# Kernel optimization log

Measured on AMD Instinct MI355X. Metric: run time of the kernel, lower is better.

Reference implementation:

```python
import jax, jax.numpy as jnp
import numpy as np

N, E, D, G, C = 50000, 800000, 128, 64, 2
SCALE = 1.0 / np.sqrt(D).astype(np.float32)


def setup_inputs() -> dict:
    key = jax.random.key(0)
    ks = jax.random.split(key, 32)
    inp = {
        "x": jax.random.normal(ks[0], (N, D), dtype=jnp.float32),
        "edge_index": jax.random.randint(ks[1], (2, E), 0, N),
        "batch": jnp.sort(jax.random.randint(ks[2], (N,), 0, G)),
    }
    i = 3
    for l in range(2):
        for nm in ("Wq", "Wk", "Wv", "Ws"):
            inp[f"{nm}{l}"] = jax.random.normal(ks[i], (D, D), dtype=jnp.float32) * 0.05
            i += 1
        for nm in ("bq", "bk", "bv", "bs"):
            inp[f"{nm}{l}"] = jnp.zeros((D,), dtype=jnp.float32)
    inp["Wc1"] = jax.random.normal(ks[i], (D // 2, D), dtype=jnp.float32) * 0.05
    inp["bc1"] = jnp.zeros((D // 2,), dtype=jnp.float32)
    inp["Wc2"] = jax.random.normal(ks[i + 1], (C, D // 2), dtype=jnp.float32) * 0.05
    inp["bc2"] = jnp.zeros((C,), dtype=jnp.float32)
    return inp


def _transformer_conv(x, src, dst, Wq, bq, Wk, bk, Wv, bv, Ws, bs):
    # PyG TransformerConv, heads=1, concat=True, root_weight=True, beta=False.
    q = x @ Wq.T + bq            # [N, D] node-level projections, then gather per edge
    k = x @ Wk.T + bk
    v = x @ Wv.T + bv
    alpha = jnp.sum(q[dst] * k[src], axis=-1) * SCALE          # [E]
    # segment softmax over incoming edges of each target node
    m = jax.ops.segment_max(alpha, dst, num_segments=N)         # [N]
    ea = jnp.exp(alpha - m[dst])
    denom = jax.ops.segment_sum(ea, dst, num_segments=N)        # [N]
    w = ea / denom[dst]                                         # [E]
    out = jax.ops.segment_sum(v[src] * w[:, None], dst, num_segments=N)  # [N, D]
    return out + x @ Ws.T + bs   # skip connection (lin_skip)


def reference(x, edge_index, batch,
              Wq0, bq0, Wk0, bk0, Wv0, bv0, Ws0, bs0,
              Wq1, bq1, Wk1, bk1, Wv1, bv1, Ws1, bs1,
              Wc1, bc1, Wc2, bc2):
    src, dst = edge_index[0], edge_index[1]
    h = _transformer_conv(x, src, dst, Wq0, bq0, Wk0, bk0, Wv0, bv0, Ws0, bs0)
    h = jax.nn.relu(h)  # dropout is a no-op in eval mode
    h = _transformer_conv(h, src, dst, Wq1, bq1, Wk1, bk1, Wv1, bv1, Ws1, bs1)
    h = jax.nn.relu(h)
    # global mean pool over graphs
    sums = jax.ops.segment_sum(h, batch, num_segments=G)        # [G, D]
    cnts = jax.ops.segment_sum(jnp.ones((h.shape[0],), h.dtype), batch, num_segments=G)
    pooled = sums / jnp.maximum(cnts, 1.0)[:, None]
    # classifier MLP: [D -> D//2 -> C]
    z = jax.nn.relu(pooled @ Wc1.T + bc1)
    return z @ Wc2.T + bc2
```

## Files before the change

### kernel.cpp

```cpp
#include <hip/hip_runtime.h>
#include <math.h>

typedef __bf16 bf16x8 __attribute__((ext_vector_type(8)));
typedef float  f32x4  __attribute__((ext_vector_type(4)));
typedef float  f32x2  __attribute__((ext_vector_type(2)));
typedef unsigned short ushort_t;
typedef unsigned short ushort8 __attribute__((ext_vector_type(8)));

constexpr int Nn = 50000;
constexpr int Ee = 800000;
constexpr int Dd = 128;
constexpr int Gg = 64;
constexpr float SCALE = 0.08838834764831845f;
constexpr float QS    = 16.0f;
constexpr float ISC   = SCALE / (QS * QS);

constexpr int CPAD = 16;

__device__ inline ushort_t f2bf(float f) {
    unsigned u = __float_as_uint(f);
    unsigned r = (u + 0x7FFF + ((u >> 16) & 1)) >> 16;
    return (ushort_t)r;
}
__device__ inline float bf2f(ushort_t b) { return __uint_as_float(((unsigned)b) << 16); }

__device__ inline char q_i8(float f) {
    int v = (int)rintf(f * QS);
    v = max(-127, min(127, v));
    return (char)v;
}

__device__ inline int xcd_group(int b, int n) {
    int q = n >> 3, r = n & 7;
    int xcd = b & 7, idx = b >> 3;
    int base = (xcd < r) ? xcd * (q + 1) : r * (q + 1) + (xcd - r) * q;
    return base + idx;
}


constexpr int EB8 = (Ee + 2047) / 2048;
constexpr int NBD = (Nn + 255) / 256;
constexpr int CWB = 64;
constexpr int N8  = Nn * Dd / 8;
constexpr int CXB = N8 / 256;

__global__ __launch_bounds__(256) void prep_kernel(
    const int* __restrict__ dst, int* __restrict__ counts, int* __restrict__ rank,
    const int* __restrict__ batch, int* __restrict__ startg, int* __restrict__ endg,
    const float* w0, const float* w1, const float* w2, const float* w3,
    const float* w4, const float* w5, const float* w6, const float* w7,
    ushort_t* __restrict__ Wfh, ushort_t* __restrict__ Wfl,
    const float* __restrict__ x, ushort_t* __restrict__ Xh, ushort_t* __restrict__ Xl) {
    int b = blockIdx.x;
    if (b < EB8) {
        int e0 = (b * 256 + threadIdx.x) * 8;
        if (e0 >= Ee) return;
        int4 d0 = *(const int4*)(dst + e0);
        int4 d1 = *(const int4*)(dst + e0 + 4);
        int r0 = atomicAdd(&counts[d0.x * CPAD], 1);
        int r1 = atomicAdd(&counts[d0.y * CPAD], 1);
        int r2 = atomicAdd(&counts[d0.z * CPAD], 1);
        int r3 = atomicAdd(&counts[d0.w * CPAD], 1);
        int r4 = atomicAdd(&counts[d1.x * CPAD], 1);
        int r5 = atomicAdd(&counts[d1.y * CPAD], 1);
        int r6 = atomicAdd(&counts[d1.z * CPAD], 1);
        int r7 = atomicAdd(&counts[d1.w * CPAD], 1);
        *(int4*)(rank + e0)     = (int4){r0, r1, r2, r3};
        *(int4*)(rank + e0 + 4) = (int4){r4, r5, r6, r7};
    } else if (b < EB8 + NBD) {
        int n = (b - EB8) * 256 + threadIdx.x;
        if (n >= Nn) return;
        int g = batch[n];
        if (n == Nn - 1 || batch[n + 1] != g) endg[g] = n + 1;
        if (n == 0 || batch[n - 1] != g) startg[g] = n;
    } else if (b < EB8 + NBD + CWB) {
        const float* ws[8] = {w0, w1, w2, w3, w4, w5, w6, w7};
        int b2 = b - (EB8 + NBD);
        int m = b2 >> 3;
        int tt = (b2 & 7) * 256 + threadIdx.x;
        int lane = tt & 63;
        int ln = lane & 15, quad = lane >> 4;
        int n = (tt >> 9) * 32 + ((tt >> 8) & 1) * 16 + ln;
        int k0 = ((tt >> 6) & 3) * 32 + quad * 8;
        const float* srcp = ws[m] + n * 128 + k0;
        float4 a = *(const float4*)(srcp);
        float4 bb = *(const float4*)(srcp + 4);
        float e[8] = {a.x, a.y, a.z, a.w, bb.x, bb.y, bb.z, bb.w};
        ushort8 h, l;
#pragma unroll
        for (int j = 0; j < 8; ++j) {
            h[j] = f2bf(e[j]);
            l[j] = f2bf(e[j] - bf2f(h[j]));
        }
        size_t o = (size_t)m * 16384 + (size_t)tt * 8;
        *(ushort8*)(Wfh + o) = h;
        *(ushort8*)(Wfl + o) = l;
    } else {
        int i = (b - (EB8 + NBD + CWB)) * 256 + threadIdx.x;
        if (i >= N8) return;
        float4 xa = ((const float4*)x)[i * 2];
        float4 xb = ((const float4*)x)[i * 2 + 1];
        float e[8] = {xa.x, xa.y, xa.z, xa.w, xb.x, xb.y, xb.z, xb.w};
        ushort8 h, l;
#pragma unroll
        for (int j = 0; j < 8; ++j) {
            h[j] = f2bf(e[j]);
            l[j] = f2bf(e[j] - bf2f(h[j]));
        }
        ((ushort8*)Xh)[i] = h;
        ((ushort8*)Xl)[i] = l;
    }
}


__global__ __launch_bounds__(256) void scan1_kernel(const int* __restrict__ counts,
                                                    int* __restrict__ offsets,
                                                    int* __restrict__ blockSums) {
    __shared__ int sh[256];
    int i = blockIdx.x * 256 + threadIdx.x;
    int v = (i < Nn) ? counts[i * CPAD] : 0;
    sh[threadIdx.x] = v;
    __syncthreads();
    for (int off = 1; off < 256; off <<= 1) {
        int t = (threadIdx.x >= off) ? sh[threadIdx.x - off] : 0;
        __syncthreads();
        sh[threadIdx.x] += t;
        __syncthreads();
    }
    if (i < Nn) offsets[i] = sh[threadIdx.x] - v;
    if (threadIdx.x == 255) blockSums[blockIdx.x] = sh[255];
}

__global__ __launch_bounds__(256) void scan2_kernel(int* __restrict__ blockSums, int nb) {
    __shared__ int sh[256];
    int t = threadIdx.x;
    int v = (t < nb) ? blockSums[t] : 0;
    sh[t] = v;
    __syncthreads();
    for (int off = 1; off < 256; off <<= 1) {
        int u = (t >= off) ? sh[t - off] : 0;
        __syncthreads();
        sh[t] += u;
        __syncthreads();
    }
    if (t < nb) blockSums[t] = sh[t] - v;
}


constexpr int XS = 136;
constexpr int NT = (Nn + 127) / 128;

__device__ __attribute__((always_inline)) void gemm_body(int bx, int which,
    const ushort_t* __restrict__ Xh, const ushort_t* __restrict__ Xl,
    const ushort_t* __restrict__ Wfh, const ushort_t* __restrict__ Wfl,
    int lw,
    const float* __restrict__ b0, const float* __restrict__ b1,
    const float* __restrict__ b2, const float* __restrict__ b3,
    char* __restrict__ Oq, char* __restrict__ Okv,
    ushort_t* __restrict__ Os) {
    __shared__ ushort_t XhS[32 * XS];
    __shared__ ushort_t XlS[32 * XS];
    const ushort_t* wfh = Wfh + (size_t)(lw + which) * 16384;
    const ushort_t* wfl = Wfl + (size_t)(lw + which) * 16384;
    const float* bias = (which == 0) ? b0 : (which == 1) ? b1 : (which == 2) ? b2 : b3;
    char* O8 = (which == 0) ? Oq : (which == 1) ? Okv : Okv + 128;
    int   o8str = (which == 0) ? 128 : 256;

    int w = threadIdx.x >> 6;
    int lane = threadIdx.x & 63;
    int quad = lane >> 4, ln = lane & 15;
    int n0 = w * 32;

    bf16x8 bh[2][4], bl[2][4];
#pragma unroll
    for (int ct = 0; ct < 2; ++ct)
#pragma unroll
        for (int kc = 0; kc < 4; ++kc) {
            int off = (w * 512 + ct * 256 + kc * 64 + lane) * 8;
            bh[ct][kc] = *(const bf16x8*)(wfh + off);
            bl[ct][kc] = *(const bf16x8*)(wfl + off);
        }
    float bias0 = bias[n0 + ln];
    float bias1 = bias[n0 + 16 + ln];

    int rowBase = bx * 128;
    int trow = threadIdx.x >> 4;
    int tcol = (threadIdx.x & 15) * 8;

    for (int chunk = 0; chunk < 4; ++chunk) {
        int cbase = rowBase + chunk * 32;
        __syncthreads();
#pragma unroll
        for (int rr = 0; rr < 2; ++rr) {
            int lrow = trow + rr * 16;
            int grow = min(cbase + lrow, Nn - 1);
            *(ushort8*)(&XhS[lrow * XS + tcol]) =
                *(const ushort8*)(Xh + (size_t)grow * 128 + tcol);
            *(ushort8*)(&XlS[lrow * XS + tcol]) =
                *(const ushort8*)(Xl + (size_t)grow * 128 + tcol);
        }
        __syncthreads();

#pragma unroll
        for (int rt = 0; rt < 2; ++rt) {
            const ushort_t* ph = &XhS[(rt * 16 + ln) * XS + quad * 8];
            const ushort_t* pl = &XlS[(rt * 16 + ln) * XS + quad * 8];
            bf16x8 ah[4], al[4];
#pragma unroll
            for (int kc = 0; kc < 4; ++kc) {
                ah[kc] = *(const bf16x8*)(ph + kc * 32);
                al[kc] = *(const bf16x8*)(pl + kc * 32);
            }
            f32x4 acc00 = {0.f,0.f,0.f,0.f}, acc01 = {0.f,0.f,0.f,0.f};
            f32x4 acc10 = {0.f,0.f,0.f,0.f}, acc11 = {0.f,0.f,0.f,0.f};
#pragma unroll
            for (int kc = 0; kc < 2; ++kc) {
                int k2 = kc + 2;
                acc00 = __builtin_amdgcn_mfma_f32_16x16x32_bf16(ah[kc], bh[0][kc], acc00, 0, 0, 0);
                acc01 = __builtin_amdgcn_mfma_f32_16x16x32_bf16(ah[kc], bh[1][kc], acc01, 0, 0, 0);
                acc10 = __builtin_amdgcn_mfma_f32_16x16x32_bf16(ah[k2], bh[0][k2], acc10, 0, 0, 0);
                acc11 = __builtin_amdgcn_mfma_f32_16x16x32_bf16(ah[k2], bh[1][k2], acc11, 0, 0, 0);
                acc00 = __builtin_amdgcn_mfma_f32_16x16x32_bf16(ah[kc], bl[0][kc], acc00, 0, 0, 0);
                acc01 = __builtin_amdgcn_mfma_f32_16x16x32_bf16(ah[kc], bl[1][kc], acc01, 0, 0, 0);
                acc10 = __builtin_amdgcn_mfma_f32_16x16x32_bf16(ah[k2], bl[0][k2], acc10, 0, 0, 0);
                acc11 = __builtin_amdgcn_mfma_f32_16x16x32_bf16(ah[k2], bl[1][k2], acc11, 0, 0, 0);
                acc00 = __builtin_amdgcn_mfma_f32_16x16x32_bf16(al[kc], bh[0][kc], acc00, 0, 0, 0);
                acc01 = __builtin_amdgcn_mfma_f32_16x16x32_bf16(al[kc], bh[1][kc], acc01, 0, 0, 0);
                acc10 = __builtin_amdgcn_mfma_f32_16x16x32_bf16(al[k2], bh[0][k2], acc10, 0, 0, 0);
                acc11 = __builtin_amdgcn_mfma_f32_16x16x32_bf16(al[k2], bh[1][k2], acc11, 0, 0, 0);
            }
            int m0 = cbase + rt * 16;
            int orow0 = m0 + quad * 4;
            bool full = (orow0 + 3) < Nn;
#pragma unroll
            for (int reg = 0; reg < 4; ++reg) {
                int orow = orow0 + reg;
                if (full || orow < Nn) {
                    float o0 = acc00[reg] + acc10[reg] + bias0;
                    float o1 = acc01[reg] + acc11[reg] + bias1;
                    if (which <= 1) {
                        size_t ob = (size_t)orow * o8str;
                        O8[ob + n0 + ln]      = q_i8(o0);
                        O8[ob + n0 + 16 + ln] = q_i8(o1);
                    } else if (which == 2) {
                        int pk = __builtin_amdgcn_cvt_pk_fp8_f32(o0, o1, 0, false);
                        size_t ob = (size_t)orow * 256;
                        O8[ob + n0 + ln]      = (char)(pk & 0xff);
                        O8[ob + n0 + 16 + ln] = (char)((pk >> 8) & 0xff);
                    } else {
                        size_t ob = (size_t)orow * 128;
                        Os[ob + n0 + ln]      = f2bf(o0);
                        Os[ob + n0 + 16 + ln] = f2bf(o1);
                    }
                }
            }
        }
    }
}

__global__ __launch_bounds__(256) void gemm_mfma_kernel(
    const ushort_t* __restrict__ Xh, const ushort_t* __restrict__ Xl,
    const ushort_t* __restrict__ Wfh, const ushort_t* __restrict__ Wfl,
    int lw,
    const float* __restrict__ b0, const float* __restrict__ b1,
    const float* __restrict__ b2, const float* __restrict__ b3,
    char* __restrict__ Oq, char* __restrict__ Okv,
    ushort_t* __restrict__ Os) {
    int wi = xcd_group(blockIdx.x, NT * 4);
    gemm_body(wi >> 2, wi & 3, Xh, Xl, Wfh, Wfl, lw, b0, b1, b2, b3, Oq, Okv, Os);
}

constexpr int G0B = NT * 4;
constexpr int EB4 = (Ee + 1023) / 1024;

__global__ __launch_bounds__(256) void gemm0_scatter_kernel(
    const ushort_t* __restrict__ Xh, const ushort_t* __restrict__ Xl,
    const ushort_t* __restrict__ Wfh, const ushort_t* __restrict__ Wfl,
    const float* __restrict__ b0, const float* __restrict__ b1,
    const float* __restrict__ b2, const float* __restrict__ b3,
    char* __restrict__ Oq, char* __restrict__ Okv, ushort_t* __restrict__ Os,
    const int* __restrict__ src, const int* __restrict__ dst,
    const int* __restrict__ offsets, const int* __restrict__ rank,
    const int* __restrict__ blockSums,
    int* __restrict__ sorted_src) {
    int b = blockIdx.x;
    if (b >= G0B) {
        int e0 = ((b - G0B) * 256 + threadIdx.x) * 4;
        if (e0 >= Ee) return;
        int4 d = *(const int4*)(dst + e0);
        int4 r = *(const int4*)(rank + e0);
        int4 s = *(const int4*)(src + e0);
        int o0 = offsets[d.x] + blockSums[d.x >> 8];
        int o1 = offsets[d.y] + blockSums[d.y >> 8];
        int o2 = offsets[d.z] + blockSums[d.z >> 8];
        int o3 = offsets[d.w] + blockSums[d.w >> 8];
        sorted_src[o0 + r.x] = s.x;
        sorted_src[o1 + r.y] = s.y;
        sorted_src[o2 + r.z] = s.z;
        sorted_src[o3 + r.w] = s.w;
        return;
    }
    int wi = xcd_group(b, G0B);
    gemm_body(wi >> 2, wi & 3, Xh, Xl, Wfh, Wfl, 0, b0, b1, b2, b3, Oq, Okv, Os);
}


__global__ __launch_bounds__(256) void attn_kernel(const char* __restrict__ q,
                                                   const char* __restrict__ kv,
                                                   const ushort_t* __restrict__ s,
                                                   const int* __restrict__ offsets,
                                                   const int* __restrict__ blockSums,
                                                   const int* __restrict__ sorted_src,
                                                   ushort_t* __restrict__ oh,
                                                   ushort_t* __restrict__ ol,
                                                   int write_split) {
    __shared__ float merge[4][8][128];
    int warp = threadIdx.x >> 6;
    int wid = blockIdx.x * 4 + warp;
    if (wid >= Nn) return;
    int lane = threadIdx.x & 63;
    int g = lane >> 3;
    int gl = lane & 7;
    int4 qw = *(const int4*)(q + (size_t)wid * 128 + gl * 16);
    int beg = offsets[wid] + blockSums[wid >> 8];
    int end = (wid == Nn - 1) ? Ee
                              : offsets[wid + 1] + blockSums[(wid + 1) >> 8];

    float l = 0.f;
    f32x4 accq[4];
#pragma unroll
    for (int j = 0; j < 4; ++j) accq[j] = (f32x4){0.f, 0.f, 0.f, 0.f};
    f32x2* acc = (f32x2*)accq;

    int e = beg + g;
    int s0 = (e < end) ? sorted_src[e] : 0;
    int s1 = (e + 8 < end) ? sorted_src[e + 8] : 0;
    const char* kvp0 = kv + (size_t)s0 * 256 + gl * 16;
    int4 kw = *(const int4*)(kvp0);
    int4 vw = *(const int4*)(kvp0 + 128);

    for (; e < end; e += 8) {
        const char* kvp1 = kv + (size_t)s1 * 256 + gl * 16;
        int4 kw1 = *(const int4*)(kvp1);
        int4 vw1 = *(const int4*)(kvp1 + 128);
        int s2 = (e + 16 < end) ? sorted_src[e + 16] : 0;

        int di = __builtin_amdgcn_sdot4(qw.x, kw.x, 0, false);
        di = __builtin_amdgcn_sdot4(qw.y, kw.y, di, false);
        di = __builtin_amdgcn_sdot4(qw.z, kw.z, di, false);
        di = __builtin_amdgcn_sdot4(qw.w, kw.w, di, false);
        di += __shfl_xor(di, 1, 64);
        di += __shfl_xor(di, 2, 64);
        di += __shfl_xor(di, 4, 64);
        float pw = __expf((float)di * ISC);
        l += pw;
        f32x2 pw2 = {pw, pw};
        {
            f32x2 lo, hi;
            lo = __builtin_amdgcn_cvt_pk_f32_fp8(vw.x, false);
            hi = __builtin_amdgcn_cvt_pk_f32_fp8(vw.x, true);
            acc[0] += pw2 * lo; acc[1] += pw2 * hi;
            lo = __builtin_amdgcn_cvt_pk_f32_fp8(vw.y, false);
            hi = __builtin_amdgcn_cvt_pk_f32_fp8(vw.y, true);
            acc[2] += pw2 * lo; acc[3] += pw2 * hi;
            lo = __builtin_amdgcn_cvt_pk_f32_fp8(vw.z, false);
            hi = __builtin_amdgcn_cvt_pk_f32_fp8(vw.z, true);
            acc[4] += pw2 * lo; acc[5] += pw2 * hi;
            lo = __builtin_amdgcn_cvt_pk_f32_fp8(vw.w, false);
            hi = __builtin_amdgcn_cvt_pk_f32_fp8(vw.w, true);
            acc[6] += pw2 * lo; acc[7] += pw2 * hi;
        }
        kw = kw1; vw = vw1; s1 = s2;
    }

    float* mrow = &merge[warp][g][gl * 16];
    *(f32x4*)(mrow + 0)  = accq[0];
    *(f32x4*)(mrow + 4)  = accq[1];
    *(f32x4*)(mrow + 8)  = accq[2];
    *(f32x4*)(mrow + 12) = accq[3];
    __builtin_amdgcn_sched_barrier(0);
    asm volatile("s_waitcnt lgkmcnt(0)" ::: "memory");
    __builtin_amdgcn_sched_barrier(0);

    l += __shfl_xor(l, 8, 64);
    l += __shfl_xor(l, 16, 64);
    l += __shfl_xor(l, 32, 64);

    int d0 = lane << 1;
    f32x2 sum = {0.f, 0.f};
#pragma unroll
    for (int gg = 0; gg < 8; ++gg) sum += *(f32x2*)(&merge[warp][gg][d0]);

    float inv = (l > 0.f) ? (1.0f / l) : 0.f;
    ushort2 sv = *(const ushort2*)(s + (size_t)wid * 128 + d0);
    float o0 = fmaxf(sum.x * inv + bf2f(sv.x), 0.f);
    float o1 = fmaxf(sum.y * inv + bf2f(sv.y), 0.f);
    ushort2 h;
    h.x = f2bf(o0); h.y = f2bf(o1);
    *(ushort2*)(oh + (size_t)wid * 128 + d0) = h;
    if (write_split) {
        ushort2 lo2;
        lo2.x = f2bf(o0 - bf2f(h.x));
        lo2.y = f2bf(o1 - bf2f(h.y));
        *(ushort2*)(ol + (size_t)wid * 128 + d0) = lo2;
    }
}


__global__ __launch_bounds__(256) void pool_kernel(const ushort_t* __restrict__ hb,
                                                   const int* __restrict__ batch,
                                                   float* __restrict__ pooled) {
    __shared__ float ps[4][128];
    int n0 = blockIdx.x * 256;
    int t = threadIdx.x;
    int lane32 = t & 31, rowgrp = t >> 5;
    for (int i = t; i < 512; i += 256) ((float*)ps)[i] = 0.f;
    __syncthreads();
    int gfirst = batch[min(n0, Nn - 1)];
    int d0 = lane32 * 4;
    float a0 = 0.f, a1 = 0.f, a2 = 0.f, a3 = 0.f;
    int curg = -1;
    for (int rr = 0; rr < 32; ++rr) {
        int n = n0 + rowgrp + rr * 8;
        if (n >= Nn) break;
        int g = batch[n];
        if (g != curg) {
            if (curg >= 0) {
                int slot = curg - gfirst;
                if (slot < 4) {
                    atomicAdd(&ps[slot][d0],     a0);
                    atomicAdd(&ps[slot][d0 + 1], a1);
                    atomicAdd(&ps[slot][d0 + 2], a2);
                    atomicAdd(&ps[slot][d0 + 3], a3);
                } else {
                    atomicAdd(&pooled[curg * Dd + d0],     a0);
                    atomicAdd(&pooled[curg * Dd + d0 + 1], a1);
                    atomicAdd(&pooled[curg * Dd + d0 + 2], a2);
                    atomicAdd(&pooled[curg * Dd + d0 + 3], a3);
                }
                a0 = a1 = a2 = a3 = 0.f;
            }
            curg = g;
        }
        ushort4 hv = *(const ushort4*)(hb + (size_t)n * 128 + d0);
        a0 += bf2f(hv.x); a1 += bf2f(hv.y); a2 += bf2f(hv.z); a3 += bf2f(hv.w);
    }
    if (curg >= 0) {
        int slot = curg - gfirst;
        if (slot < 4) {
            atomicAdd(&ps[slot][d0],     a0);
            atomicAdd(&ps[slot][d0 + 1], a1);
            atomicAdd(&ps[slot][d0 + 2], a2);
            atomicAdd(&ps[slot][d0 + 3], a3);
        } else {
            atomicAdd(&pooled[curg * Dd + d0],     a0);
            atomicAdd(&pooled[curg * Dd + d0 + 1], a1);
            atomicAdd(&pooled[curg * Dd + d0 + 2], a2);
            atomicAdd(&pooled[curg * Dd + d0 + 3], a3);
        }
    }
    __syncthreads();
    int glast = batch[min(n0 + 255, Nn - 1)];
    int nslots = min(glast - gfirst + 1, 4);
    for (int i = t; i < nslots * 128; i += 256) {
        int slot = i >> 7, d = i & 127;
        atomicAdd(&pooled[(gfirst + slot) * Dd + d], ps[slot][d]);
    }
}

__global__ __launch_bounds__(64) void mlp_kernel(const float* __restrict__ pooled,
                                                 const int* __restrict__ startg,
                                                 const int* __restrict__ endg,
                                                 const float* __restrict__ Wc1,
                                                 const float* __restrict__ bc1,
                                                 const float* __restrict__ Wc2,
                                                 const float* __restrict__ bc2,
                                                 float* __restrict__ out) {
    __shared__ float pm[128];
    __shared__ float hid[64];
    int g = blockIdx.x, t = threadIdx.x;
    float cnt = fmaxf((float)(endg[g] - startg[g]), 1.0f);
    float invc = 1.0f / cnt;
    pm[t]      = pooled[g * 128 + t] * invc;
    pm[t + 64] = pooled[g * 128 + 64 + t] * invc;
    __syncthreads();
    float acc = bc1[t];
    for (int i = 0; i < 128; ++i) acc += pm[i] * Wc1[t * 128 + i];
    hid[t] = fmaxf(acc, 0.f);
    __syncthreads();
    if (t < 2) {
        float a = bc2[t];
        for (int i = 0; i < 64; ++i) a += hid[i] * Wc2[t * 64 + i];
        out[g * 2 + t] = a;
    }
}


extern "C" void kernel_launch(void* const* d_in, const int* in_sizes, int n_in,
                              void* d_out, int out_size, void* d_ws, size_t ws_size,
                              hipStream_t stream) {
    const float* x   = (const float*)d_in[0];
    const int*   ei  = (const int*)d_in[1];
    const int* batch = (const int*)d_in[2];
    const float* W[2][4];
    const float* B[2][4];
    for (int l = 0; l < 2; ++l) {
        for (int j = 0; j < 4; ++j) W[l][j] = (const float*)d_in[3 + l * 8 + j];
        for (int j = 0; j < 4; ++j) B[l][j] = (const float*)d_in[3 + l * 8 + 4 + j];
    }
    const float* Wc1 = (const float*)d_in[19];
    const float* bc1 = (const float*)d_in[20];
    const float* Wc2 = (const float*)d_in[21];
    const float* bc2 = (const float*)d_in[22];
    float* out = (float*)d_out;

    const int* src = ei;
    const int* dst = ei + Ee;

    char* p = (char*)d_ws;
    auto alloc = [&](size_t bytes) {
        void* r = (void*)p;
        p += (bytes + 255) & ~(size_t)255;
        return r;
    };
    char*     q  = (char*)alloc((size_t)Nn * 128);
    char*     kv = (char*)alloc((size_t)Nn * 256);
    ushort_t* ss = (ushort_t*)alloc((size_t)Nn * 128 * 2);
    ushort_t* hb = (ushort_t*)alloc((size_t)Nn * 128 * 2);
    ushort_t* Xh = (ushort_t*)alloc((size_t)Nn * 128 * 2);
    ushort_t* Xl = (ushort_t*)alloc((size_t)Nn * 128 * 2);
    ushort_t* Wfh = (ushort_t*)alloc((size_t)8 * 16384 * 2);
    ushort_t* Wfl = (ushort_t*)alloc((size_t)8 * 16384 * 2);
    char* zbase = p;
    int*   counts = (int*)alloc((size_t)Nn * CPAD * 4);
    int*   startg = (int*)alloc(Gg * 4);
    int*   endg   = (int*)alloc(Gg * 4);
    float* pooled = (float*)alloc(Gg * Dd * 4);
    size_t zbytes = (size_t)(p - zbase);
    int* offsets    = (int*)alloc((size_t)(Nn + 1) * 4);
    int* rank       = (int*)alloc((size_t)Ee * 4);
    int* blockSums  = (int*)alloc(256 * 4);
    int* sorted_src = (int*)alloc((size_t)Ee * 4);

    hipMemsetAsync(zbase, 0, zbytes, stream);

    constexpr int NB = (Nn + 255) / 256;

    prep_kernel<<<EB8 + NBD + CWB + CXB, 256, 0, stream>>>(
        dst, counts, rank, batch, startg, endg,
        W[0][0], W[0][1], W[0][2], W[0][3], W[1][0], W[1][1], W[1][2], W[1][3],
        Wfh, Wfl, x, Xh, Xl);
    scan1_kernel<<<NB, 256, 0, stream>>>(counts, offsets, blockSums);
    scan2_kernel<<<1, 256, 0, stream>>>(blockSums, NB);

    gemm0_scatter_kernel<<<G0B + EB4, 256, 0, stream>>>(
        Xh, Xl, Wfh, Wfl, B[0][0], B[0][1], B[0][2], B[0][3],
        q, kv, ss, src, dst, offsets, rank, blockSums, sorted_src);

    attn_kernel<<<(Nn + 3) / 4, 256, 0, stream>>>(q, kv, ss, offsets, blockSums,
                                                  sorted_src, Xh, Xl, 1);
    gemm_mfma_kernel<<<NT * 4, 256, 0, stream>>>(Xh, Xl, Wfh, Wfl, 4,
                                                 B[1][0], B[1][1], B[1][2], B[1][3],
                                                 q, kv, ss);
    attn_kernel<<<(Nn + 3) / 4, 256, 0, stream>>>(q, kv, ss, offsets, blockSums,
                                                  sorted_src, hb, hb, 0);

    pool_kernel<<<(Nn + 255) / 256, 256, 0, stream>>>(hb, batch, pooled);
    mlp_kernel<<<Gg, 64, 0, stream>>>(pooled, startg, endg, Wc1, bc1, Wc2, bc2, out);
}
```

Baseline: 298.5 us.

## Process two destination nodes per wavefront in attention kernel

Each 64-lane wavefront is split into two 32-lane halves, each handling its own destination node with 4 edge groups instead of 8. This halves the block count and is meant to cut the idle lanes and reduction overhead on low-degree nodes, since the average degree is 16. The price is less edge-level parallelism per node and a longer serial loop on high-degree nodes. The bounds check on the node index is removed, which relies on N being divisible by 8.

```diff
diff --git a/kernel.cpp b/kernel.cpp
--- a/kernel.cpp
+++ b/kernel.cpp
@@ -314,13 +314,14 @@
                                                    ushort_t* __restrict__ oh,
                                                    ushort_t* __restrict__ ol,
                                                    int write_split) {
-    __shared__ float merge[4][8][128];
+    __shared__ float merge[4][2][4][128];
     int warp = threadIdx.x >> 6;
-    int wid = blockIdx.x * 4 + warp;
-    if (wid >= Nn) return;
     int lane = threadIdx.x & 63;
-    int g = lane >> 3;
-    int gl = lane & 7;
+    int half = lane >> 5;
+    int l5 = lane & 31;
+    int g = l5 >> 3;
+    int gl = l5 & 7;
+    int wid = blockIdx.x * 8 + warp * 2 + half;
     int4 qw = *(const int4*)(q + (size_t)wid * 128 + gl * 16);
     int beg = offsets[wid] + blockSums[wid >> 8];
     int end = (wid == Nn - 1) ? Ee
@@ -334,16 +335,16 @@
 
     int e = beg + g;
     int s0 = (e < end) ? sorted_src[e] : 0;
-    int s1 = (e + 8 < end) ? sorted_src[e + 8] : 0;
+    int s1 = (e + 4 < end) ? sorted_src[e + 4] : 0;
     const char* kvp0 = kv + (size_t)s0 * 256 + gl * 16;
     int4 kw = *(const int4*)(kvp0);
     int4 vw = *(const int4*)(kvp0 + 128);
 
-    for (; e < end; e += 8) {
+    for (; e < end; e += 4) {
         const char* kvp1 = kv + (size_t)s1 * 256 + gl * 16;
         int4 kw1 = *(const int4*)(kvp1);
         int4 vw1 = *(const int4*)(kvp1 + 128);
-        int s2 = (e + 16 < end) ? sorted_src[e + 16] : 0;
+        int s2 = (e + 8 < end) ? sorted_src[e + 8] : 0;
 
         int di = __builtin_amdgcn_sdot4(qw.x, kw.x, 0, false);
         di = __builtin_amdgcn_sdot4(qw.y, kw.y, di, false);
@@ -373,7 +374,7 @@
         kw = kw1; vw = vw1; s1 = s2;
     }
 
-    float* mrow = &merge[warp][g][gl * 16];
+    float* mrow = &merge[warp][half][g][gl * 16];
     *(f32x4*)(mrow + 0)  = accq[0];
     *(f32x4*)(mrow + 4)  = accq[1];
     *(f32x4*)(mrow + 8)  = accq[2];
@@ -384,25 +385,29 @@
 
     l += __shfl_xor(l, 8, 64);
     l += __shfl_xor(l, 16, 64);
-    l += __shfl_xor(l, 32, 64);
-
-    int d0 = lane << 1;
-    f32x2 sum = {0.f, 0.f};
-#pragma unroll
-    for (int gg = 0; gg < 8; ++gg) sum += *(f32x2*)(&merge[warp][gg][d0]);
+
+    int d0 = l5 << 2;
+    f32x4 sum = {0.f, 0.f, 0.f, 0.f};
+#pragma unroll
+    for (int gg = 0; gg < 4; ++gg) sum += *(f32x4*)(&merge[warp][half][gg][d0]);
 
     float inv = (l > 0.f) ? (1.0f / l) : 0.f;
-    ushort2 sv = *(const ushort2*)(s + (size_t)wid * 128 + d0);
-    float o0 = fmaxf(sum.x * inv + bf2f(sv.x), 0.f);
-    float o1 = fmaxf(sum.y * inv + bf2f(sv.y), 0.f);
-    ushort2 h;
-    h.x = f2bf(o0); h.y = f2bf(o1);
-    *(ushort2*)(oh + (size_t)wid * 128 + d0) = h;
+    ushort4 sv = *(const ushort4*)(s + (size_t)wid * 128 + d0);
+    float o[4];
+    o[0] = fmaxf(sum[0] * inv + bf2f(sv.x), 0.f);
+    o[1] = fmaxf(sum[1] * inv + bf2f(sv.y), 0.f);
+    o[2] = fmaxf(sum[2] * inv + bf2f(sv.z), 0.f);
+    o[3] = fmaxf(sum[3] * inv + bf2f(sv.w), 0.f);
+    ushort4 h;
+    h.x = f2bf(o[0]); h.y = f2bf(o[1]); h.z = f2bf(o[2]); h.w = f2bf(o[3]);
+    *(ushort4*)(oh + (size_t)wid * 128 + d0) = h;
     if (write_split) {
-        ushort2 lo2;
-        lo2.x = f2bf(o0 - bf2f(h.x));
-        lo2.y = f2bf(o1 - bf2f(h.y));
-        *(ushort2*)(ol + (size_t)wid * 128 + d0) = lo2;
+        ushort4 lo4;
+        lo4.x = f2bf(o[0] - bf2f(h.x));
+        lo4.y = f2bf(o[1] - bf2f(h.y));
+        lo4.z = f2bf(o[2] - bf2f(h.z));
+        lo4.w = f2bf(o[3] - bf2f(h.w));
+        *(ushort4*)(ol + (size_t)wid * 128 + d0) = lo4;
     }
 }
 
@@ -557,13 +562,13 @@
         Xh, Xl, Wfh, Wfl, B[0][0], B[0][1], B[0][2], B[0][3],
         q, kv, ss, src, dst, offsets, rank, blockSums, sorted_src);
 
-    attn_kernel<<<(Nn + 3) / 4, 256, 0, stream>>>(q, kv, ss, offsets, blockSums,
-                                                  sorted_src, Xh, Xl, 1);
+    attn_kernel<<<Nn / 8, 256, 0, stream>>>(q, kv, ss, offsets, blockSums,
+                                            sorted_src, Xh, Xl, 1);
     gemm_mfma_kernel<<<NT * 4, 256, 0, stream>>>(Xh, Xl, Wfh, Wfl, 4,
                                                  B[1][0], B[1][1], B[1][2], B[1][3],
                                                  q, kv, ss);
-    attn_kernel<<<(Nn + 3) / 4, 256, 0, stream>>>(q, kv, ss, offsets, blockSums,
-                                                  sorted_src, hb, hb, 0);
+    attn_kernel<<<Nn / 8, 256, 0, stream>>>(q, kv, ss, offsets, blockSums,
+                                            sorted_src, hb, hb, 0);
 
     pool_kernel<<<(Nn + 255) / 256, 256, 0, stream>>>(hb, batch, pooled);
     mlp_kernel<<<Gg, 64, 0, stream>>>(pooled, startg, endg, Wc1, bc1, Wc2, bc2, out);
```

Result: no change. 297.2 us (-0.5%).
